# Optimization experiments

Hardware: AMD Instinct MI355X
Metric: run time of the kernel (lower is better)

Reference implementation:

```python
import jax, jax.numpy as jnp
import numpy as np

# DualAttention dims
D_MODEL = 1024
H_SA = 8          # self-attention heads
H_RA = 8          # relational-attention heads
TOTAL_H = H_SA + H_RA
HEAD_DIM = D_MODEL // TOTAL_H   # 64
KEY_DIM = HEAD_DIM              # 64
N_REL = 8
REL_PROJ = HEAD_DIM * H_RA // N_REL  # 64
B, S = 2, 2048


def apply_rope(x, cos, sin):
    # x: [b, s, h, d]; cos/sin: [s, d//2]. Pairs are (0,1),(2,3),... as in
    # llama-style apply_rotary_emb (reshape(..., -1, 2).unbind(-1)).
    xr, xi = x[..., 0::2], x[..., 1::2]
    c = cos[None, :, None, :]
    s_ = sin[None, :, None, :]
    out = jnp.stack([xr * c - xi * s_, xr * s_ + xi * c], axis=-1)
    return out.reshape(x.shape)


def setup_inputs() -> dict:
    key = jax.random.key(0)
    ks = jax.random.split(key, 16)
    def w(k, shape):
        return jax.random.normal(k, shape, jnp.float32) * 0.02
    x = jax.random.normal(ks[0], (B, S, D_MODEL), jnp.float32)
    symbols = jax.random.normal(ks[1], (B, S, D_MODEL), jnp.float32)
    # real RoPE tables
    pos = np.arange(S, dtype=np.float32)[:, None]
    inv = 1.0 / (10000.0 ** (np.arange(0, KEY_DIM, 2, dtype=np.float32) / KEY_DIM))
    ang = pos * inv[None, :]
    freqs_cos = jnp.asarray(np.cos(ang), jnp.float32)
    freqs_sin = jnp.asarray(np.sin(ang), jnp.float32)
    return dict(
        x=x, symbols=symbols, freqs_cos=freqs_cos, freqs_sin=freqs_sin,
        # self-attention branch (torch Linear weights: [out, in])
        wq_sa=w(ks[2], (H_SA * KEY_DIM, D_MODEL)),
        wk_sa=w(ks[3], (H_SA * KEY_DIM, D_MODEL)),
        wv_sa=w(ks[4], (H_SA * HEAD_DIM, D_MODEL)),
        wo_sa=w(ks[5], (H_SA * HEAD_DIM, H_SA * HEAD_DIM)),
        # relational-attention branch
        wq_attn=w(ks[6], (H_RA * KEY_DIM, D_MODEL)),
        wk_attn=w(ks[7], (H_RA * KEY_DIM, D_MODEL)),
        wq_rel=w(ks[8], (N_REL * REL_PROJ, D_MODEL)),
        wk_rel=w(ks[9], (N_REL * REL_PROJ, D_MODEL)),
        wr=w(ks[10], (H_RA, HEAD_DIM, N_REL)),
        wv_ra=w(ks[11], (H_RA * HEAD_DIM, D_MODEL)),
        wo_ra=w(ks[12], (H_RA * HEAD_DIM, H_RA * HEAD_DIM)),
    )


def reference(x, symbols, freqs_cos, freqs_sin,
              wq_sa, wk_sa, wv_sa, wo_sa,
              wq_attn, wk_attn, wq_rel, wk_rel, wr, wv_ra, wo_ra):
    b, s, _ = x.shape
    attn_scale = 1.0 / np.sqrt(HEAD_DIM).astype(np.float32)
    rel_scale = 1.0 / np.sqrt(REL_PROJ).astype(np.float32)
    causal = jnp.tril(jnp.ones((s, s), dtype=bool))
    neg = jnp.finfo(x.dtype).min

    def heads(t, h, d):
        return t.reshape(b, s, h, d)

    # ---- self-attention branch (causal SDPA with RoPE) ----
    q = apply_rope(heads(x @ wq_sa.T, H_SA, KEY_DIM), freqs_cos, freqs_sin)
    k = apply_rope(heads(x @ wk_sa.T, H_SA, KEY_DIM), freqs_cos, freqs_sin)
    v = heads(x @ wv_sa.T, H_SA, HEAD_DIM)
    scores = jnp.einsum('bihd,bjhd->bhij', q, k) * attn_scale
    a = jax.nn.softmax(jnp.where(causal, scores, neg), axis=-1)
    sa_out = jnp.einsum('bhij,bjhd->bihd', a, v).reshape(b, s, H_SA * HEAD_DIM) @ wo_sa.T

    # ---- relational-attention branch ----
    # attention scores (softmax selection), with RoPE
    qa = apply_rope(heads(x @ wq_attn.T, H_RA, KEY_DIM), freqs_cos, freqs_sin)
    ka = apply_rope(heads(x @ wk_attn.T, H_RA, KEY_DIM), freqs_cos, freqs_sin)
    ra_scores = jnp.einsum('bihd,bjhd->bhij', qa, ka) * attn_scale
    alpha = jax.nn.softmax(jnp.where(causal, ra_scores, neg), axis=-1)
    # relations r(x_i, x_j) in R^{N_REL} (identity rel_activation)
    qr = heads(x @ wq_rel.T, N_REL, REL_PROJ)
    kr = heads(x @ wk_rel.T, N_REL, REL_PROJ)
    rel = jnp.einsum('birp,bjrp->brij', qr, kr) * rel_scale  # [b, R, i, j]
    # symbol values: wv applied to retrieved symbols
    sv = heads(symbols @ wv_ra.T, H_RA, HEAD_DIM)
    attended_sym = jnp.einsum('bhij,bjhd->bihd', alpha, sv)          # [b, i, h, d]
    attended_rel = jnp.einsum('bhij,brij->bihr', alpha, rel)         # [b, i, h, R]
    rel_out = jnp.einsum('bihr,hdr->bihd', attended_rel, wr)
    ra_out = (attended_sym + rel_out).reshape(b, s, H_RA * HEAD_DIM) @ wo_ra.T

    # DualAttention: concat branch outputs along feature dim -> [b, s, d_model]
    return jnp.concatenate([sa_out, ra_out], axis=-1)
```

## Files before the change

kernel.cpp:

```cpp
#include <hip/hip_runtime.h>

#define B_   2
#define S_   2048
#define H_   8
#define D_   64
#define DM_  1024
#define PJ_  512
#define NT_  32
#define NTRI 528
#define NCHK 80

typedef short bf16x8 __attribute__((ext_vector_type(8)));
typedef float f32x4 __attribute__((ext_vector_type(4)));

__device__ __forceinline__ float bf2f(unsigned int u) {
  return __uint_as_float(u << 16);
}
__device__ __forceinline__ unsigned short f2bf(float f) {
  unsigned int u = __float_as_uint(f);
  u += 0x7fffu + ((u >> 16) & 1u);
  return (unsigned short)(u >> 16);
}

__device__ __forceinline__ void glds16(const unsigned short* g, unsigned short* l) {
  __builtin_amdgcn_global_load_lds(
      (const __attribute__((address_space(1))) void*)g,
      (__attribute__((address_space(3))) void*)l, 16, 0, 0);
}

struct CvtJobs {
  const float*    src[12];
  unsigned short* dst[12];
  int             n4[12];
};

__global__ __launch_bounds__(256) void cvt_many(CvtJobs J) {
  const int j = blockIdx.y;
  const int i = blockIdx.x * 256 + threadIdx.x;
  if (i >= J.n4[j]) return;
  const float4 v = ((const float4*)J.src[j])[i];
  ushort4 o;
  o.x = f2bf(v.x); o.y = f2bf(v.y); o.z = f2bf(v.z); o.w = f2bf(v.w);
  ((ushort4*)J.dst[j])[i] = o;
}

__device__ __forceinline__
void gemm128_glds(const unsigned short* __restrict__ A, int m0,
                  const unsigned short* __restrict__ Wb,
                  unsigned short* __restrict__ Cb, int ldc, int KD,
                  unsigned short* As, unsigned short* Bs)
{
  const int tid = threadIdx.x;
  const int wv = tid >> 6, lane = tid & 63;
  const int r15 = lane & 15, quad = lane >> 4;
  const int wm = (wv >> 1) * 64, wn = (wv & 1) * 64;
  f32x4 acc[4][4];
#pragma unroll
  for (int i = 0; i < 4; ++i)
#pragma unroll
    for (int j = 0; j < 4; ++j) acc[i][j] = (f32x4){0.f, 0.f, 0.f, 0.f};

  const int srow = wv * 16 + (lane >> 2);
  const int scol = ((lane & 3) ^ ((lane >> 3) & 3)) * 8;
  const unsigned short* gaA0 = A + (size_t)(m0 + srow) * KD + scol;
  const unsigned short* gaA1 = gaA0 + (size_t)64 * KD;
  const unsigned short* gaB0 = Wb + (size_t)srow * KD + scol;
  const unsigned short* gaB1 = gaB0 + (size_t)64 * KD;
  unsigned short* ldsA0 = As + wv * 512;
  unsigned short* ldsA1 = As + 2048 + wv * 512;
  unsigned short* ldsB0 = Bs + wv * 512;
  unsigned short* ldsB1 = Bs + 2048 + wv * 512;
  const int rxor = (r15 >> 1) & 3;

  for (int kk = 0; kk < KD; kk += 32) {
    __syncthreads();
    glds16(gaA0 + kk, ldsA0);
    glds16(gaA1 + kk, ldsA1);
    glds16(gaB0 + kk, ldsB0);
    glds16(gaB1 + kk, ldsB1);
    __syncthreads();
    bf16x8 af[4], bf[4];
#pragma unroll
    for (int i = 0; i < 4; ++i)
      af[i] = *(const bf16x8*)(As + (wm + i * 16 + r15) * 32 + ((quad ^ rxor) << 3));
#pragma unroll
    for (int j = 0; j < 4; ++j)
      bf[j] = *(const bf16x8*)(Bs + (wn + j * 16 + r15) * 32 + ((quad ^ rxor) << 3));
#pragma unroll
    for (int i = 0; i < 4; ++i)
#pragma unroll
      for (int j = 0; j < 4; ++j)
        acc[i][j] = __builtin_amdgcn_mfma_f32_16x16x32_bf16(af[i], bf[j], acc[i][j], 0, 0, 0);
  }
#pragma unroll
  for (int i = 0; i < 4; ++i)
#pragma unroll
    for (int r = 0; r < 4; ++r) {
      unsigned short* cp = Cb + (size_t)(wm + i * 16 + quad * 4 + r) * ldc + wn + r15;
#pragma unroll
      for (int j = 0; j < 4; ++j) cp[j * 16] = f2bf(acc[i][j][r]);
    }
}

__global__ __launch_bounds__(256)
void proj_tiled(const unsigned short* __restrict__ XB,
                const unsigned short* __restrict__ SYB,
                const unsigned short* __restrict__ Wcat,
                unsigned short* __restrict__ Qbase,
                unsigned short* __restrict__ SV)
{
  __shared__ unsigned short As[128 * 32];
  __shared__ unsigned short Bs[128 * 32];
  const int m0 = blockIdx.x * 128;
  const int ny = blockIdx.y;
  const size_t NB = (size_t)B_ * S_ * PJ_;
  const unsigned short* A;
  const unsigned short* Wb;
  unsigned short* Cb;
  if (ny < 28) {
    const int n0 = ny * 128;
    A  = XB;
    Wb = Wcat + (size_t)n0 * DM_;
    Cb = Qbase + (size_t)(n0 >> 9) * NB + (size_t)m0 * PJ_ + (n0 & 511);
  } else {
    const int n0 = (ny - 28) * 128;
    A  = SYB;
    Wb = Wcat + (size_t)7 * PJ_ * DM_ + (size_t)n0 * DM_;
    Cb = SV + (size_t)m0 * PJ_ + n0;
  }
  gemm128_glds(A, m0, Wb, Cb, PJ_, DM_, As, Bs);
}

__global__ __launch_bounds__(256)
void out_tiled(const unsigned short* __restrict__ Asa,
               const unsigned short* __restrict__ Ara,
               const unsigned short* __restrict__ WOSA,
               const unsigned short* __restrict__ WORA,
               float* __restrict__ Out)
{
  __shared__ unsigned short As[128 * 40];
  __shared__ unsigned short Bs[64 * 40];
  const int m0 = blockIdx.x * 128;
  const int ny = blockIdx.y;
  const int n0 = (ny & 7) * 64;
  const unsigned short* A  = (ny < 8) ? Asa : Ara;
  const unsigned short* Wb = ((ny < 8) ? WOSA : WORA) + (size_t)n0 * PJ_;
  float* Cb = Out + (size_t)m0 * DM_ + ((ny < 8) ? 0 : 512) + n0;

  const int tid = threadIdx.x;
  const int wv = tid >> 6, lane = tid & 63;
  const int r15 = lane & 15, quad = lane >> 4;
  const int wm = wv * 32;
  f32x4 acc[2][4];
#pragma unroll
  for (int i = 0; i < 2; ++i)
#pragma unroll
    for (int j = 0; j < 4; ++j) acc[i][j] = (f32x4){0.f, 0.f, 0.f, 0.f};

  const int arow = tid >> 1, ac = (tid & 1) * 16;
  const int brow = tid >> 2, bc = (tid & 3) * 8;
  const unsigned short* ga = A + (size_t)(m0 + arow) * PJ_ + ac;
  const unsigned short* gb = Wb + (size_t)brow * PJ_ + bc;
  unsigned short* la = As + arow * 40 + ac;
  unsigned short* lb = Bs + brow * 40 + bc;

  for (int kk = 0; kk < PJ_; kk += 32) {
    __syncthreads();
    const uint4 a0 = *(const uint4*)(ga + kk);
    const uint4 a1 = *(const uint4*)(ga + kk + 8);
    const uint4 b0 = *(const uint4*)(gb + kk);
    *(uint4*)la       = a0;
    *(uint4*)(la + 8) = a1;
    *(uint4*)lb       = b0;
    __syncthreads();
    bf16x8 af[2], bf[4];
#pragma unroll
    for (int i = 0; i < 2; ++i)
      af[i] = *(const bf16x8*)(As + (wm + i * 16 + r15) * 40 + quad * 8);
#pragma unroll
    for (int j = 0; j < 4; ++j)
      bf[j] = *(const bf16x8*)(Bs + (j * 16 + r15) * 40 + quad * 8);
#pragma unroll
    for (int i = 0; i < 2; ++i)
#pragma unroll
      for (int j = 0; j < 4; ++j)
        acc[i][j] = __builtin_amdgcn_mfma_f32_16x16x32_bf16(af[i], bf[j], acc[i][j], 0, 0, 0);
  }
#pragma unroll
  for (int i = 0; i < 2; ++i)
#pragma unroll
    for (int r = 0; r < 4; ++r) {
      float* cp = Cb + (size_t)(wm + i * 16 + quad * 4 + r) * DM_ + r15;
#pragma unroll
      for (int j = 0; j < 4; ++j) cp[j * 16] = acc[i][j][r];
    }
}

__global__ __launch_bounds__(256)
void rel_rope(const unsigned short* __restrict__ QRg, const unsigned short* __restrict__ KRg,
              unsigned short* __restrict__ RelCF,
              unsigned short* __restrict__ Qp, unsigned short* __restrict__ Kp,
              unsigned short* __restrict__ QAp, unsigned short* __restrict__ KAp,
              const float* __restrict__ fcp, const float* __restrict__ fsp)
{
  __shared__ unsigned short As[128 * 72];
  __shared__ unsigned short Bs[128 * 72];
  const int t = blockIdx.x;
  int I = 0;
  while ((I + 1) * (I + 2) / 2 <= t) ++I;
  const int J = t - I * (I + 1) / 2;
  const int rr = blockIdx.y & 7, b = blockIdx.y >> 3;
  const int tid = threadIdx.x;
  const int wv = tid >> 6, lane = tid & 63;
  const int r15 = lane & 15, quad = lane >> 4;

  const int srow = tid >> 1, c32 = (tid & 1) * 32;
  const unsigned short* ga = QRg + (size_t)(b * S_ + I * 128 + srow) * PJ_ + rr * 64 + c32;
  const unsigned short* gb = KRg + (size_t)(b * S_ + J * 128 + srow) * PJ_ + rr * 64 + c32;
  unsigned short* la = As + srow * 72 + c32;
  unsigned short* lb = Bs + srow * 72 + c32;
#pragma unroll
  for (int q = 0; q < 4; ++q) {
    *(uint4*)(la + q * 8) = *(const uint4*)(ga + q * 8);
    *(uint4*)(lb + q * 8) = *(const uint4*)(gb + q * 8);
  }
  __syncthreads();

  const int wm = (wv >> 1) * 64, wn = (wv & 1) * 64;
  const int it64 = 2 * I + (wv >> 1), jt64 = 2 * J + (wv & 1);
  if (jt64 <= it64) {
    f32x4 acc[4][4];
#pragma unroll
    for (int i = 0; i < 4; ++i)
#pragma unroll
      for (int j = 0; j < 4; ++j) acc[i][j] = (f32x4){0.f, 0.f, 0.f, 0.f};
#pragma unroll
    for (int k0 = 0; k0 < 2; ++k0) {
      bf16x8 af[4], bf[4];
#pragma unroll
      for (int i = 0; i < 4; ++i)
        af[i] = *(const bf16x8*)(As + (wm + i * 16 + r15) * 72 + quad * 8 + k0 * 32);
#pragma unroll
      for (int j = 0; j < 4; ++j)
        bf[j] = *(const bf16x8*)(Bs + (wn + j * 16 + r15) * 72 + quad * 8 + k0 * 32);
#pragma unroll
      for (int i = 0; i < 4; ++i)
#pragma unroll
        for (int j = 0; j < 4; ++j)
          acc[i][j] = __builtin_amdgcn_mfma_f32_16x16x32_bf16(af[i], bf[j], acc[i][j], 0, 0, 0);
    }
    unsigned short* out = RelCF + ((size_t)(b * 8 + rr) * NTRI + (size_t)it64 * (it64 + 1) / 2 + jt64) * 4096;
#pragma unroll
    for (int i = 0; i < 4; ++i) {
      unsigned short tmp[16];
#pragma unroll
      for (int j = 0; j < 4; ++j)
#pragma unroll
        for (int r = 0; r < 4; ++r)
          tmp[j * 4 + r] = f2bf(acc[i][j][r] * 0.125f);
      unsigned short* op = out + (size_t)(i * 64 + lane) * 16;
      *(uint4*)op       = *(const uint4*)tmp;
      *(uint4*)(op + 8) = *(const uint4*)(tmp + 8);
    }
  }

  const int bid = (int)blockIdx.y * 136 + (int)blockIdx.x;
  const int gt = bid * 256 + tid;
#pragma unroll
  for (int k = 0; k < 2; ++k) {
    const int i = gt * 2 + k;
    if (i >= 4 * 262144) continue;
    const int tn = i >> 18;
    const int r2 = i & 262143;
    unsigned short* P = (tn == 0) ? Qp : (tn == 1) ? Kp : (tn == 2) ? QAp : KAp;
    const int b2 = r2 >> 17;
    const int s2 = (r2 >> 6) & 2047;
    const int c8 = (r2 & 63) * 8;
    const int ci0 = (c8 & 63) >> 1;
    const size_t off2 = ((size_t)(b2 * S_ + s2)) * PJ_ + c8;
    uint4 v = *(const uint4*)(P + off2);
    unsigned int u[4] = {v.x, v.y, v.z, v.w};
    unsigned int o[4];
#pragma unroll
    for (int q = 0; q < 4; ++q) {
      const float xr = __uint_as_float(u[q] << 16);
      const float xi = __uint_as_float(u[q] & 0xffff0000u);
      const float cs = fcp[s2 * 32 + ci0 + q];
      const float sn = fsp[s2 * 32 + ci0 + q];
      const unsigned short lo = f2bf(xr * cs - xi * sn);
      const unsigned short hi = f2bf(xr * sn + xi * cs);
      o[q] = (unsigned int)lo | ((unsigned int)hi << 16);
    }
    uint4 ov; ov.x = o[0]; ov.y = o[1]; ov.z = o[2]; ov.w = o[3];
    *(uint4*)(P + off2) = ov;
  }
}

__global__ __launch_bounds__(256)
void flash_part(const unsigned short* __restrict__ Qsa, const unsigned short* __restrict__ Ksa,
                const unsigned short* __restrict__ Vsa,
                const unsigned short* __restrict__ Qra, const unsigned short* __restrict__ Kra,
                const unsigned short* __restrict__ SVra,
                const unsigned short* __restrict__ RelCF,
                unsigned short* __restrict__ PoP, float* __restrict__ lP,
                float* __restrict__ arpP)
{
  __shared__ unsigned short Ks[2][64][72];
  __shared__ unsigned short Vt[2][64][72];
  __shared__ unsigned short Ps[64][72];
  const int x = blockIdx.x;
  int it, c;
  if (x < 8)       { it = x;                    c = 0; }
  else if (x < 24) { it = 8 + ((x - 8) >> 1);   c = (x - 8) & 1; }
  else if (x < 48) { it = 16 + (x - 24) / 3;    c = (x - 24) % 3; }
  else             { it = 24 + ((x - 48) >> 2); c = (x - 48) & 3; }
  const int j0 = c * 8;
  const int jend = (j0 + 8 < it + 1) ? (j0 + 8) : (it + 1);
  const bool ra = (blockIdx.y >= 8);
  const int h = blockIdx.y & 7;
  const int b = blockIdx.z;
  const int chunkId = (b * 16 + (int)blockIdx.y) * NCHK + x;
  const unsigned short* Qg = ra ? Qra : Qsa;
  const unsigned short* Kg = ra ? Kra : Ksa;
  const unsigned short* Vg = ra ? SVra : Vsa;
  const int tid = threadIdx.x;
  const int wv = tid >> 6, lane = tid & 63;
  const int r15 = lane & 15, quad = lane >> 4;
  const size_t bh = (size_t)b * S_ * PJ_ + (size_t)h * D_;
  const size_t relStride = (size_t)NTRI * 4096;

  const int kr0 = tid >> 3, kc0 = (tid & 7) << 3;
  const int kr1 = (tid + 256) >> 3;
  const unsigned short* kgp = Kg + bh + kc0;
  const unsigned short* vgp = Vg + bh + (size_t)lane * PJ_ + wv * 8;

  const unsigned short* qp = Qg + bh + (size_t)(it * 64 + wv * 16 + r15) * PJ_ + quad * 8;
  const bf16x8 aq0 = *(const bf16x8*)qp;
  const bf16x8 aq1 = *(const bf16x8*)(qp + 32);

  unsigned short one8[8];
#pragma unroll
  for (int i = 0; i < 8; ++i) one8[i] = 0x3F80;
  const bf16x8 ones = *(const bf16x8*)one8;

  f32x4 o_acc[4];
  f32x4 l_acc = {0.f, 0.f, 0.f, 0.f};
  float arp[4][8];
#pragma unroll
  for (int n = 0; n < 4; ++n) o_acc[n] = (f32x4){0.f, 0.f, 0.f, 0.f};
#pragma unroll
  for (int r = 0; r < 4; ++r)
#pragma unroll
    for (int rr = 0; rr < 8; ++rr) arp[r][rr] = 0.f;
  const int row0 = it * 64 + wv * 16 + quad * 4;
  const size_t relTileBase = (size_t)(b * 8) * NTRI * 4096
                           + (size_t)(it * (it + 1)) / 2 * 4096
                           + (size_t)(wv * 64 + lane) * 16;

  uint4 ka0, ka1, va0, va1;
  {
    const size_t jb = (size_t)j0 * 64 * PJ_;
    ka0 = *(const uint4*)(kgp + jb + (size_t)kr0 * PJ_);
    ka1 = *(const uint4*)(kgp + jb + (size_t)kr1 * PJ_);
    va0 = *(const uint4*)(vgp + jb);
    va1 = *(const uint4*)(vgp + jb + 32);
  }
  int p = 0;
  {
    *(uint4*)&Ks[0][kr0][kc0] = ka0;
    *(uint4*)&Ks[0][kr1][kc0] = ka1;
    unsigned short t8[8];
    *(uint4*)t8 = va0;
#pragma unroll
    for (int m = 0; m < 8; ++m) Vt[0][wv * 8 + m][lane] = t8[m];
    *(uint4*)t8 = va1;
#pragma unroll
    for (int m = 0; m < 8; ++m) Vt[0][wv * 8 + 32 + m][lane] = t8[m];
  }
  __syncthreads();

  for (int jt = j0; jt < jend; ++jt) {
    const bool more = (jt + 1 < jend);
    if (more) {
      const size_t jb = (size_t)(jt + 1) * 64 * PJ_;
      ka0 = *(const uint4*)(kgp + jb + (size_t)kr0 * PJ_);
      ka1 = *(const uint4*)(kgp + jb + (size_t)kr1 * PJ_);
      va0 = *(const uint4*)(vgp + jb);
      va1 = *(const uint4*)(vgp + jb + 32);
    }
    uint4 pre[8];
    const unsigned short* rtBase = RelCF + relTileBase + (size_t)jt * 4096;
    if (ra) {
      const unsigned short* rt = rtBase;
#pragma unroll
      for (int q = 0; q < 4; ++q) {
        pre[2 * q]     = *(const uint4*)rt;
        pre[2 * q + 1] = *(const uint4*)(rt + 8);
        rt += relStride;
      }
    }
    f32x4 s[4];
#pragma unroll
    for (int n = 0; n < 4; ++n) s[n] = (f32x4){0.f, 0.f, 0.f, 0.f};
#pragma unroll
    for (int k0 = 0; k0 < 2; ++k0) {
      const bf16x8 af = k0 ? aq1 : aq0;
#pragma unroll
      for (int n = 0; n < 4; ++n) {
        const bf16x8 bf = *(const bf16x8*)&Ks[p][n * 16 + r15][quad * 8 + k0 * 32];
        s[n] = __builtin_amdgcn_mfma_f32_16x16x32_bf16(af, bf, s[n], 0, 0, 0);
      }
    }
    if (jt == it) {
#pragma unroll
      for (int n = 0; n < 4; ++n)
#pragma unroll
        for (int r = 0; r < 4; ++r) {
          const bool ok = (jt * 64 + n * 16 + r15 <= row0 + r);
          s[n][r] = ok ? __expf(s[n][r] * 0.125f - 4.0f) : 0.f;
        }
    } else {
#pragma unroll
      for (int n = 0; n < 4; ++n)
#pragma unroll
        for (int r = 0; r < 4; ++r)
          s[n][r] = __expf(s[n][r] * 0.125f - 4.0f);
    }
#pragma unroll
    for (int n = 0; n < 4; ++n)
#pragma unroll
      for (int r = 0; r < 4; ++r)
        Ps[wv * 16 + quad * 4 + r][n * 16 + r15] = f2bf(s[n][r]);
    if (ra) {
      const unsigned short* rt2 = rtBase + 4 * relStride;
#pragma unroll
      for (int rr = 0; rr < 8; ++rr) {
        unsigned int ru[8];
        if (rr < 4) {
          *(uint4*)ru       = pre[2 * rr];
          *(uint4*)(ru + 4) = pre[2 * rr + 1];
        } else {
          *(uint4*)ru       = *(const uint4*)rt2;
          *(uint4*)(ru + 4) = *(const uint4*)(rt2 + 8);
          rt2 += relStride;
        }
#pragma unroll
        for (int n = 0; n < 4; ++n) {
          const unsigned int u0 = ru[2 * n], u1 = ru[2 * n + 1];
          arp[0][rr] += s[n][0] * __uint_as_float(u0 << 16);
          arp[1][rr] += s[n][1] * __uint_as_float(u0 & 0xffff0000u);
          arp[2][rr] += s[n][2] * __uint_as_float(u1 << 16);
          arp[3][rr] += s[n][3] * __uint_as_float(u1 & 0xffff0000u);
        }
      }
    }
#pragma unroll
    for (int k0 = 0; k0 < 2; ++k0) {
      const bf16x8 pf = *(const bf16x8*)&Ps[wv * 16 + r15][quad * 8 + k0 * 32];
#pragma unroll
      for (int n = 0; n < 4; ++n) {
        const bf16x8 vf = *(const bf16x8*)&Vt[p][n * 16 + r15][quad * 8 + k0 * 32];
        o_acc[n] = __builtin_amdgcn_mfma_f32_16x16x32_bf16(pf, vf, o_acc[n], 0, 0, 0);
      }
      l_acc = __builtin_amdgcn_mfma_f32_16x16x32_bf16(pf, ones, l_acc, 0, 0, 0);
    }
    if (more) {
      const int q = p ^ 1;
      *(uint4*)&Ks[q][kr0][kc0] = ka0;
      *(uint4*)&Ks[q][kr1][kc0] = ka1;
      unsigned short t8[8];
      *(uint4*)t8 = va0;
#pragma unroll
      for (int m = 0; m < 8; ++m) Vt[q][wv * 8 + m][lane] = t8[m];
      *(uint4*)t8 = va1;
#pragma unroll
      for (int m = 0; m < 8; ++m) Vt[q][wv * 8 + 32 + m][lane] = t8[m];
      __syncthreads();
      p = q;
    }
  }
  unsigned short* po = PoP + (size_t)chunkId * 4096;
#pragma unroll
  for (int n = 0; n < 4; ++n)
#pragma unroll
    for (int r = 0; r < 4; ++r)
      po[(wv * 16 + quad * 4 + r) * 64 + n * 16 + r15] = f2bf(o_acc[n][r]);
  if (r15 == 0) {
#pragma unroll
    for (int r = 0; r < 4; ++r)
      lP[(size_t)chunkId * 64 + wv * 16 + quad * 4 + r] = l_acc[r];
  }
  if (ra) {
#pragma unroll
    for (int r = 0; r < 4; ++r)
#pragma unroll
      for (int rr = 0; rr < 8; ++rr)
#pragma unroll
        for (int o = 1; o < 16; o <<= 1)
          arp[r][rr] += __shfl_xor(arp[r][rr], o);
    if (r15 == 0) {
#pragma unroll
      for (int r = 0; r < 4; ++r) {
        float* ap = arpP + (size_t)chunkId * 512 + (wv * 16 + quad * 4 + r) * 8;
#pragma unroll
        for (int rr = 0; rr < 8; ++rr) ap[rr] = arp[r][rr];
      }
    }
  }
}

__global__ __launch_bounds__(256)
void flash_merge(const unsigned short* __restrict__ PoP, const float* __restrict__ lP,
                 const float* __restrict__ arpP, const float* __restrict__ wrF,
                 unsigned short* __restrict__ Osa, unsigned short* __restrict__ Ora)
{
  const int it = blockIdx.x;
  const int hh = blockIdx.y;
  const int b  = blockIdx.z;
  const bool ra = (hh >= 8);
  const int h = hh & 7;
  const int nc = it / 8 + 1;
  int cb;
  if (it < 8)       cb = it;
  else if (it < 16) cb = 8 + 2 * (it - 8);
  else if (it < 24) cb = 24 + 3 * (it - 16);
  else              cb = 48 + 4 * (it - 24);
  const int cid0 = (b * 16 + hh) * NCHK + cb;
  const int tid = threadIdx.x;
  const int row = tid >> 2;
  const int cg  = tid & 3;

  float L = 0.f;
  for (int c = 0; c < nc; ++c) L += lP[(size_t)(cid0 + c) * 64 + row];
  const float inv = 1.f / L;

  float o[16];
#pragma unroll
  for (int k = 0; k < 16; ++k) o[k] = 0.f;
  for (int c = 0; c < nc; ++c) {
    const unsigned short* pp = PoP + (size_t)(cid0 + c) * 4096 + row * 64 + cg * 16;
    unsigned int u[8];
    *(uint4*)u       = *(const uint4*)pp;
    *(uint4*)(u + 4) = *(const uint4*)(pp + 8);
#pragma unroll
    for (int q = 0; q < 8; ++q) {
      o[2 * q]     += __uint_as_float(u[q] << 16);
      o[2 * q + 1] += __uint_as_float(u[q] & 0xffff0000u);
    }
  }
  if (ra) {
    float A[8];
#pragma unroll
    for (int rr = 0; rr < 8; ++rr) A[rr] = 0.f;
    for (int c = 0; c < nc; ++c) {
      const float* ap = arpP + (size_t)(cid0 + c) * 512 + row * 8;
#pragma unroll
      for (int rr = 0; rr < 8; ++rr) A[rr] += ap[rr];
    }
#pragma unroll
    for (int k = 0; k < 16; ++k) {
      const float* wp = wrF + ((size_t)h * 64 + cg * 16 + k) * 8;
      float ro = 0.f;
#pragma unroll
      for (int rr = 0; rr < 8; ++rr) ro += A[rr] * wp[rr];
      o[k] += ro;
    }
  }
  const size_t bh = (size_t)b * S_ * PJ_ + (size_t)h * D_;
  unsigned short* op = (ra ? Ora : Osa) + bh + (size_t)(it * 64 + row) * PJ_ + cg * 16;
#pragma unroll
  for (int k = 0; k < 16; ++k) op[k] = f2bf(o[k] * inv);
}

extern "C" void kernel_launch(void* const* d_in, const int* in_sizes, int n_in,
                              void* d_out, int out_size, void* d_ws, size_t ws_size,
                              hipStream_t stream)
{
  (void)in_sizes; (void)n_in; (void)out_size; (void)ws_size;
  const float* x    = (const float*)d_in[0];
  const float* sym  = (const float*)d_in[1];
  const float* fc   = (const float*)d_in[2];
  const float* fs   = (const float*)d_in[3];
  const float* wqsa = (const float*)d_in[4];
  const float* wksa = (const float*)d_in[5];
  const float* wvsa = (const float*)d_in[6];
  const float* wosa = (const float*)d_in[7];
  const float* wqat = (const float*)d_in[8];
  const float* wkat = (const float*)d_in[9];
  const float* wqre = (const float*)d_in[10];
  const float* wkre = (const float*)d_in[11];
  const float* wr   = (const float*)d_in[12];
  const float* wvra = (const float*)d_in[13];
  const float* wora = (const float*)d_in[14];

  unsigned short* wsb = (unsigned short*)d_ws;
  const size_t NX = (size_t)B_ * S_ * DM_;
  const size_t NB = (size_t)B_ * S_ * PJ_;
  const size_t NW = (size_t)PJ_ * DM_;
  const size_t NO = (size_t)PJ_ * PJ_;
  const size_t NR = (size_t)B_ * 8 * NTRI * 4096;
  const size_t NCH = (size_t)B_ * 16 * NCHK;

  size_t off = 0;
  unsigned short* XB   = wsb + off; off += NX;
  unsigned short* SYB  = wsb + off; off += NX;
  unsigned short* WB[8];
  for (int i = 0; i < 8; ++i) { WB[i] = wsb + off; off += NW; }
  unsigned short* WOSA = wsb + off; off += NO;
  unsigned short* WORA = wsb + off; off += NO;
  unsigned short* Q    = wsb + off; off += NB;
  unsigned short* K    = wsb + off; off += NB;
  unsigned short* V    = wsb + off; off += NB;
  unsigned short* QA   = wsb + off; off += NB;
  unsigned short* KA   = wsb + off; off += NB;
  unsigned short* QR   = wsb + off; off += NB;
  unsigned short* KR   = wsb + off; off += NB;
  unsigned short* SV   = wsb + off; off += NB;
  unsigned short* Asa  = wsb + off; off += NB;
  unsigned short* Ara  = wsb + off; off += NB;
  unsigned short* RelCF = wsb + off; off += NR;
  unsigned short* PoP  = XB;
  float* lP   = (float*)(wsb + off); off += NCH * 64 * 2;
  float* arpP = (float*)(wsb + off); off += NCH * 512 * 2;

  CvtJobs cj;
  cj.src[0]  = x;    cj.dst[0]  = XB;    cj.n4[0]  = (int)(NX / 4);
  cj.src[1]  = sym;  cj.dst[1]  = SYB;   cj.n4[1]  = (int)(NX / 4);
  cj.src[2]  = wqsa; cj.dst[2]  = WB[0]; cj.n4[2]  = (int)(NW / 4);
  cj.src[3]  = wksa; cj.dst[3]  = WB[1]; cj.n4[3]  = (int)(NW / 4);
  cj.src[4]  = wvsa; cj.dst[4]  = WB[2]; cj.n4[4]  = (int)(NW / 4);
  cj.src[5]  = wqat; cj.dst[5]  = WB[3]; cj.n4[5]  = (int)(NW / 4);
  cj.src[6]  = wkat; cj.dst[6]  = WB[4]; cj.n4[6]  = (int)(NW / 4);
  cj.src[7]  = wqre; cj.dst[7]  = WB[5]; cj.n4[7]  = (int)(NW / 4);
  cj.src[8]  = wkre; cj.dst[8]  = WB[6]; cj.n4[8]  = (int)(NW / 4);
  cj.src[9]  = wvra; cj.dst[9]  = WB[7]; cj.n4[9]  = (int)(NW / 4);
  cj.src[10] = wosa; cj.dst[10] = WOSA;  cj.n4[10] = (int)(NO / 4);
  cj.src[11] = wora; cj.dst[11] = WORA;  cj.n4[11] = (int)(NO / 4);
  cvt_many<<<dim3(4096, 12), dim3(256), 0, stream>>>(cj);

  proj_tiled<<<dim3(32, 32), dim3(256), 0, stream>>>(XB, SYB, WB[0], Q, SV);
  rel_rope<<<dim3(136, 16), dim3(256), 0, stream>>>(QR, KR, RelCF, Q, K, QA, KA, fc, fs);
  flash_part<<<dim3(NCHK, 16, B_), dim3(256), 0, stream>>>(
      Q, K, V, QA, KA, SV, RelCF, PoP, lP, arpP);
  flash_merge<<<dim3(NT_, 16, B_), dim3(256), 0, stream>>>(
      PoP, lP, arpP, wr, Asa, Ara);
  out_tiled<<<dim3(32, 16), dim3(256), 0, stream>>>(Asa, Ara, WOSA, WORA, (float*)d_out);
}
```

Baseline: 326.5 us.

## Compute transposed scores in flash kernel to keep P in registers

The flash kernel now computes S^T by swapping the MFMA operands, so each lane holds the scores of a single query row. P is packed straight into registers as the A operand of the PV MFMA, which removes the Ps shared-memory round trip and the ones-MFMA row sum. The V tile is written to LDS with a permuted column index to match the new k ordering. The rel tile producer also swaps its operands so the relation layout matches the transposed fragments. The arp and l reductions shrink to two shuffles, and launch bounds request 4 blocks per CU; the risk is mismatched layouts or register pressure.

```diff
diff --git a/kernel.cpp b/kernel.cpp
--- a/kernel.cpp
+++ b/kernel.cpp
@@ -231,9 +231,9 @@
   if (jt64 <= it64) {
     f32x4 acc[4][4];
 #pragma unroll
-    for (int i = 0; i < 4; ++i)
-#pragma unroll
-      for (int j = 0; j < 4; ++j) acc[i][j] = (f32x4){0.f, 0.f, 0.f, 0.f};
+    for (int a = 0; a < 4; ++a)
+#pragma unroll
+      for (int bq = 0; bq < 4; ++bq) acc[a][bq] = (f32x4){0.f, 0.f, 0.f, 0.f};
 #pragma unroll
     for (int k0 = 0; k0 < 2; ++k0) {
       bf16x8 af[4], bf[4];
@@ -244,21 +244,21 @@
       for (int j = 0; j < 4; ++j)
         bf[j] = *(const bf16x8*)(Bs + (wn + j * 16 + r15) * 72 + quad * 8 + k0 * 32);
 #pragma unroll
-      for (int i = 0; i < 4; ++i)
-#pragma unroll
-        for (int j = 0; j < 4; ++j)
-          acc[i][j] = __builtin_amdgcn_mfma_f32_16x16x32_bf16(af[i], bf[j], acc[i][j], 0, 0, 0);
+      for (int a = 0; a < 4; ++a)
+#pragma unroll
+        for (int bq = 0; bq < 4; ++bq)
+          acc[a][bq] = __builtin_amdgcn_mfma_f32_16x16x32_bf16(bf[a], af[bq], acc[a][bq], 0, 0, 0);
     }
     unsigned short* out = RelCF + ((size_t)(b * 8 + rr) * NTRI + (size_t)it64 * (it64 + 1) / 2 + jt64) * 4096;
 #pragma unroll
-    for (int i = 0; i < 4; ++i) {
+    for (int bq = 0; bq < 4; ++bq) {
       unsigned short tmp[16];
 #pragma unroll
-      for (int j = 0; j < 4; ++j)
+      for (int a = 0; a < 4; ++a)
 #pragma unroll
         for (int r = 0; r < 4; ++r)
-          tmp[j * 4 + r] = f2bf(acc[i][j][r] * 0.125f);
-      unsigned short* op = out + (size_t)(i * 64 + lane) * 16;
+          tmp[a * 4 + r] = f2bf(acc[a][bq][r] * 0.125f);
+      unsigned short* op = out + (size_t)(bq * 64 + lane) * 16;
       *(uint4*)op       = *(const uint4*)tmp;
       *(uint4*)(op + 8) = *(const uint4*)(tmp + 8);
     }
@@ -296,7 +296,7 @@
   }
 }
 
-__global__ __launch_bounds__(256)
+__global__ __launch_bounds__(256, 4)
 void flash_part(const unsigned short* __restrict__ Qsa, const unsigned short* __restrict__ Ksa,
                 const unsigned short* __restrict__ Vsa,
                 const unsigned short* __restrict__ Qra, const unsigned short* __restrict__ Kra,
@@ -307,7 +307,6 @@
 {
   __shared__ unsigned short Ks[2][64][72];
   __shared__ unsigned short Vt[2][64][72];
-  __shared__ unsigned short Ps[64][72];
   const int x = blockIdx.x;
   int it, c;
   if (x < 8)       { it = x;                    c = 0; }
@@ -333,26 +332,20 @@
   const int kr1 = (tid + 256) >> 3;
   const unsigned short* kgp = Kg + bh + kc0;
   const unsigned short* vgp = Vg + bh + (size_t)lane * PJ_ + wv * 8;
+  const int kcol = ((lane >> 2) & 3) * 8 + ((lane >> 4) & 1) * 4 + (lane & 3) + (lane >> 5) * 32;
 
   const unsigned short* qp = Qg + bh + (size_t)(it * 64 + wv * 16 + r15) * PJ_ + quad * 8;
   const bf16x8 aq0 = *(const bf16x8*)qp;
   const bf16x8 aq1 = *(const bf16x8*)(qp + 32);
 
-  unsigned short one8[8];
-#pragma unroll
-  for (int i = 0; i < 8; ++i) one8[i] = 0x3F80;
-  const bf16x8 ones = *(const bf16x8*)one8;
-
   f32x4 o_acc[4];
-  f32x4 l_acc = {0.f, 0.f, 0.f, 0.f};
-  float arp[4][8];
+  float l_row = 0.f;
+  float arp[8];
 #pragma unroll
   for (int n = 0; n < 4; ++n) o_acc[n] = (f32x4){0.f, 0.f, 0.f, 0.f};
 #pragma unroll
-  for (int r = 0; r < 4; ++r)
-#pragma unroll
-    for (int rr = 0; rr < 8; ++rr) arp[r][rr] = 0.f;
-  const int row0 = it * 64 + wv * 16 + quad * 4;
+  for (int rr = 0; rr < 8; ++rr) arp[rr] = 0.f;
+  const int il = wv * 16 + r15;
   const size_t relTileBase = (size_t)(b * 8) * NTRI * 4096
                            + (size_t)(it * (it + 1)) / 2 * 4096
                            + (size_t)(wv * 64 + lane) * 16;
@@ -372,10 +365,10 @@
     unsigned short t8[8];
     *(uint4*)t8 = va0;
 #pragma unroll
-    for (int m = 0; m < 8; ++m) Vt[0][wv * 8 + m][lane] = t8[m];
+    for (int m = 0; m < 8; ++m) Vt[0][wv * 8 + m][kcol] = t8[m];
     *(uint4*)t8 = va1;
 #pragma unroll
-    for (int m = 0; m < 8; ++m) Vt[0][wv * 8 + 32 + m][lane] = t8[m];
+    for (int m = 0; m < 8; ++m) Vt[0][wv * 8 + 32 + m][kcol] = t8[m];
   }
   __syncthreads();
 
@@ -404,11 +397,11 @@
     for (int n = 0; n < 4; ++n) s[n] = (f32x4){0.f, 0.f, 0.f, 0.f};
 #pragma unroll
     for (int k0 = 0; k0 < 2; ++k0) {
-      const bf16x8 af = k0 ? aq1 : aq0;
+      const bf16x8 bq = k0 ? aq1 : aq0;
 #pragma unroll
       for (int n = 0; n < 4; ++n) {
-        const bf16x8 bf = *(const bf16x8*)&Ks[p][n * 16 + r15][quad * 8 + k0 * 32];
-        s[n] = __builtin_amdgcn_mfma_f32_16x16x32_bf16(af, bf, s[n], 0, 0, 0);
+        const bf16x8 kf = *(const bf16x8*)&Ks[p][n * 16 + r15][quad * 8 + k0 * 32];
+        s[n] = __builtin_amdgcn_mfma_f32_16x16x32_bf16(kf, bq, s[n], 0, 0, 0);
       }
     }
     if (jt == it) {
@@ -416,7 +409,7 @@
       for (int n = 0; n < 4; ++n)
 #pragma unroll
         for (int r = 0; r < 4; ++r) {
-          const bool ok = (jt * 64 + n * 16 + r15 <= row0 + r);
+          const bool ok = (n * 16 + quad * 4 + r <= il);
           s[n][r] = ok ? __expf(s[n][r] * 0.125f - 4.0f) : 0.f;
         }
     } else {
@@ -426,11 +419,29 @@
         for (int r = 0; r < 4; ++r)
           s[n][r] = __expf(s[n][r] * 0.125f - 4.0f);
     }
-#pragma unroll
-    for (int n = 0; n < 4; ++n)
-#pragma unroll
-      for (int r = 0; r < 4; ++r)
-        Ps[wv * 16 + quad * 4 + r][n * 16 + r15] = f2bf(s[n][r]);
+    unsigned short pw[16];
+#pragma unroll
+    for (int jj = 0; jj < 8; ++jj) {
+      pw[jj]     = f2bf(s[(jj >> 2)][jj & 3]);
+      pw[8 + jj] = f2bf(s[2 + (jj >> 2)][jj & 3]);
+    }
+    const bf16x8 pa0 = *(const bf16x8*)pw;
+    const bf16x8 pa1 = *(const bf16x8*)(pw + 8);
+    {
+      float ls = 0.f;
+#pragma unroll
+      for (int jj = 0; jj < 16; ++jj) ls += bf2f((unsigned int)pw[jj]);
+      l_row += ls;
+    }
+#pragma unroll
+    for (int k0 = 0; k0 < 2; ++k0) {
+      const bf16x8 pf = k0 ? pa1 : pa0;
+#pragma unroll
+      for (int n = 0; n < 4; ++n) {
+        const bf16x8 vf = *(const bf16x8*)&Vt[p][n * 16 + r15][quad * 8 + k0 * 32];
+        o_acc[n] = __builtin_amdgcn_mfma_f32_16x16x32_bf16(pf, vf, o_acc[n], 0, 0, 0);
+      }
+    }
     if (ra) {
       const unsigned short* rt2 = rtBase + 4 * relStride;
 #pragma unroll
@@ -444,25 +455,17 @@
           *(uint4*)(ru + 4) = *(const uint4*)(rt2 + 8);
           rt2 += relStride;
         }
+        float a = arp[rr];
 #pragma unroll
         for (int n = 0; n < 4; ++n) {
           const unsigned int u0 = ru[2 * n], u1 = ru[2 * n + 1];
-          arp[0][rr] += s[n][0] * __uint_as_float(u0 << 16);
-          arp[1][rr] += s[n][1] * __uint_as_float(u0 & 0xffff0000u);
-          arp[2][rr] += s[n][2] * __uint_as_float(u1 << 16);
-          arp[3][rr] += s[n][3] * __uint_as_float(u1 & 0xffff0000u);
+          a += s[n][0] * __uint_as_float(u0 << 16);
+          a += s[n][1] * __uint_as_float(u0 & 0xffff0000u);
+          a += s[n][2] * __uint_as_float(u1 << 16);
+          a += s[n][3] * __uint_as_float(u1 & 0xffff0000u);
         }
+        arp[rr] = a;
       }
-    }
-#pragma unroll
-    for (int k0 = 0; k0 < 2; ++k0) {
-      const bf16x8 pf = *(const bf16x8*)&Ps[wv * 16 + r15][quad * 8 + k0 * 32];
-#pragma unroll
-      for (int n = 0; n < 4; ++n) {
-        const bf16x8 vf = *(const bf16x8*)&Vt[p][n * 16 + r15][quad * 8 + k0 * 32];
-        o_acc[n] = __builtin_amdgcn_mfma_f32_16x16x32_bf16(pf, vf, o_acc[n], 0, 0, 0);
-      }
-      l_acc = __builtin_amdgcn_mfma_f32_16x16x32_bf16(pf, ones, l_acc, 0, 0, 0);
     }
     if (more) {
       const int q = p ^ 1;
@@ -471,10 +474,10 @@
       unsigned short t8[8];
       *(uint4*)t8 = va0;
 #pragma unroll
-      for (int m = 0; m < 8; ++m) Vt[q][wv * 8 + m][lane] = t8[m];
+      for (int m = 0; m < 8; ++m) Vt[q][wv * 8 + m][kcol] = t8[m];
       *(uint4*)t8 = va1;
 #pragma unroll
-      for (int m = 0; m < 8; ++m) Vt[q][wv * 8 + 32 + m][lane] = t8[m];
+      for (int m = 0; m < 8; ++m) Vt[q][wv * 8 + 32 + m][kcol] = t8[m];
       __syncthreads();
       p = q;
     }
@@ -485,26 +488,20 @@
 #pragma unroll
     for (int r = 0; r < 4; ++r)
       po[(wv * 16 + quad * 4 + r) * 64 + n * 16 + r15] = f2bf(o_acc[n][r]);
-  if (r15 == 0) {
-#pragma unroll
-    for (int r = 0; r < 4; ++r)
-      lP[(size_t)chunkId * 64 + wv * 16 + quad * 4 + r] = l_acc[r];
-  }
+  l_row += __shfl_xor(l_row, 16);
+  l_row += __shfl_xor(l_row, 32);
+  if (lane < 16)
+    lP[(size_t)chunkId * 64 + wv * 16 + lane] = l_row;
   if (ra) {
 #pragma unroll
-    for (int r = 0; r < 4; ++r)
-#pragma unroll
-      for (int rr = 0; rr < 8; ++rr)
-#pragma unroll
-        for (int o = 1; o < 16; o <<= 1)
-          arp[r][rr] += __shfl_xor(arp[r][rr], o);
-    if (r15 == 0) {
-#pragma unroll
-      for (int r = 0; r < 4; ++r) {
-        float* ap = arpP + (size_t)chunkId * 512 + (wv * 16 + quad * 4 + r) * 8;
-#pragma unroll
-        for (int rr = 0; rr < 8; ++rr) ap[rr] = arp[r][rr];
-      }
+    for (int rr = 0; rr < 8; ++rr) {
+      arp[rr] += __shfl_xor(arp[rr], 16);
+      arp[rr] += __shfl_xor(arp[rr], 32);
+    }
+    if (lane < 16) {
+      float* ap = arpP + (size_t)chunkId * 512 + (wv * 16 + lane) * 8;
+#pragma unroll
+      for (int rr = 0; rr < 8; ++rr) ap[rr] = arp[rr];
     }
   }
 }
```

Measured after the change: 610.7 us. +87.0%, slower.
